# Kernel optimization log

Measured on AMD Instinct MI355X. Metric: run time of the kernel, lower is better.

## Reference

```python
import jax, jax.numpy as jnp
import numpy as np

B, C, K, D = 8192, 64, 256, 64  # batch, ncodebooks, ncentroids, subvect_len
BN_EPS = 1e-5


def setup_inputs() -> dict:
    key = jax.random.key(0)
    k1, k2 = jax.random.split(key)
    return {
        "inputs": jax.random.normal(k1, (B, C, D), dtype=jnp.float32),
        "centroids_k": jax.random.normal(k2, (C, K, D), dtype=jnp.float32) * 0.1,
        "bn_gamma": jnp.ones((C,), dtype=jnp.float32),
        "bn_beta": jnp.zeros((C,), dtype=jnp.float32),
    }


def _response(inputs, centroids_k, bn_gamma, bn_beta):
    # dot-metric scores: (B, C, K)
    r = jnp.einsum('bcd,ckd->bck', inputs, centroids_k)
    # BatchNorm1d over channel dim C (training mode: biased batch stats over B and K)
    mean = r.mean(axis=(0, 2), keepdims=True)
    var = ((r - mean) ** 2).mean(axis=(0, 2), keepdims=True)
    r = (r - mean) * jax.lax.rsqrt(var + BN_EPS)
    return r * bn_gamma[None, :, None] + bn_beta[None, :, None]


def reference(inputs, centroids_k, bn_gamma, bn_beta):
    r = _response(inputs, centroids_k, bn_gamma, bn_beta)
    # torch.max(response, -1) -> (values, indices)
    mse = r.max(axis=-1)                 # (B, C)
    codes = jnp.argmax(r, axis=-1)       # (B, C) int
    # tie_in_n_out=True: _centroids_v is _centroids_k
    return codes, mse, centroids_k
```

## Files before the change

kernel.cpp:

```cpp
#include <hip/hip_runtime.h>

#define B_  8192
#define C_  64
#define K_  256
#define D_  64
#define NBT     2
#define ROWS_BT 512
#define GX  (B_ / (ROWS_BT * NBT))
#define BC_ (B_ * C_)
#define BN_EPS 1e-5

#define WCAP_C 1024
#define DELTA  4e-3f

typedef _Float16 f16x8 __attribute__((ext_vector_type(8)));
typedef float    f32x4 __attribute__((ext_vector_type(4)));

__device__ __forceinline__ int swz(int row, int dbyte) {
    return (row * 128 + dbyte) ^ ((row & 7) << 4);
}

__device__ __forceinline__ f16x8 cvt8(const float* p) {
    float4 u0 = *(const float4*)p;
    float4 u1 = *(const float4*)(p + 4);
    return (f16x8){(_Float16)u0.x, (_Float16)u0.y, (_Float16)u0.z, (_Float16)u0.w,
                   (_Float16)u1.x, (_Float16)u1.y, (_Float16)u1.z, (_Float16)u1.w};
}

#define MERGE2(B1, S1, B2, S2)                                              \
    {                                                                       \
        const float lo_ = fminf(B1, B2);                                    \
        B1 = fmaxf(B1, B2);                                                 \
        S1 = fmaxf(lo_, fmaxf(S1, S2));                                     \
    }

__global__ __launch_bounds__(512, 4) void dpq_mfma(
    const float* __restrict__ x,
    const float* __restrict__ cent,
    const float* __restrict__ gamma,
    float* __restrict__ out,
    float* __restrict__ part_sum,
    float* __restrict__ part_sq,
    int* __restrict__ wcount,
    int* __restrict__ worklist)
{
    __shared__ char lds[32768];
    const int c   = blockIdx.y;
    const int tid = threadIdx.x;
    const float sgn = (gamma[c] < 0.0f) ? -1.0f : 1.0f;

    {
        const int row = tid >> 1, half = tid & 1;
        const float* g = cent + ((size_t)c * K_ + row) * D_ + half * 32;
#pragma unroll
        for (int q = 0; q < 4; ++q) {
            float v[8];
#pragma unroll
            for (int j = 0; j < 8; ++j) v[j] = g[q * 8 + j] * sgn;
            f16x8 h = {(_Float16)v[0], (_Float16)v[1], (_Float16)v[2], (_Float16)v[3],
                       (_Float16)v[4], (_Float16)v[5], (_Float16)v[6], (_Float16)v[7]};
            *(f16x8*)(lds + swz(row, half * 64 + q * 16)) = h;
        }
    }
    __syncthreads();

    const int wid = tid >> 6, lane = tid & 63;
    const int col = lane & 15, grp = lane >> 4;
    const unsigned g4 = (unsigned)(grp * 4);

    float taccs[4] = {0.f, 0.f, 0.f, 0.f};
    float taccq[4] = {0.f, 0.f, 0.f, 0.f};

    for (int bt = 0; bt < NBT; ++bt) {
        const int b0 = blockIdx.x * (ROWS_BT * NBT) + bt * ROWS_BT + wid * 64;

        f16x8 xfa[4], xfb[4];
        {
            const float* xb = x + ((size_t)(b0 + col) * C_ + c) * D_ + grp * 8;
            const size_t st16 = (size_t)16 * C_ * D_;
#pragma unroll
            for (int T = 0; T < 4; ++T) {
                xfa[T] = cvt8(xb + T * st16);
                xfb[T] = cvt8(xb + T * st16 + 32);
            }
        }

        float bestv[4], secv[4];
#pragma unroll
        for (int T = 0; T < 4; ++T) { bestv[T] = -3.4e38f; secv[T] = -3.4e38f; }

#pragma unroll 4
        for (int t = 0; t < 16; ++t) {
            const f16x8 a0 = *(const f16x8*)(lds + swz(t * 16 + col,      grp * 16));
            const f16x8 a1 = *(const f16x8*)(lds + swz(t * 16 + col, 64 + grp * 16));

            f32x4 p[4];
#pragma unroll
            for (int T = 0; T < 4; ++T) {
                f32x4 acc = {0.f, 0.f, 0.f, 0.f};
                acc = __builtin_amdgcn_mfma_f32_16x16x32_f16(a0, xfa[T], acc, 0, 0, 0);
                acc = __builtin_amdgcn_mfma_f32_16x16x32_f16(a1, xfb[T], acc, 0, 0, 0);
                p[T] = acc;
            }

            const unsigned kt = ((unsigned)t << 4) | g4;
#pragma unroll
            for (int j = 0; j < 4; ++j) {
                const unsigned kj = kt + j;
#pragma unroll
                for (int T = 0; T < 4; ++T) {
                    const float r = p[T][j];
                    taccs[T] += r;
                    taccq[T] = fmaf(r, r, taccq[T]);
                    const float pk = __uint_as_float(
                        (__float_as_uint(r) & 0xFFFFFF00u) | kj);
                    secv[T]  = __builtin_amdgcn_fmed3f(pk, bestv[T], secv[T]);
                    bestv[T] = fmaxf(bestv[T], pk);
                }
            }
        }

#pragma unroll
        for (int T = 0; T < 4; ++T) {
            float bv = bestv[T], sv = secv[T];
#pragma unroll
            for (int m = 16; m <= 32; m <<= 1) {
                const float ob = __shfl_xor(bv, m);
                const float os = __shfl_xor(sv, m);
                MERGE2(bv, sv, ob, os);
            }
            if (grp == 0) {
                const int b = b0 + T * 16 + col;
                const size_t idx = (size_t)b * C_ + c;
                const unsigned bits = __float_as_uint(bv);
                out[idx] = (float)(bits & 255u);
                out[(size_t)BC_ + idx] = __uint_as_float(bits & 0xFFFFFF00u);
                if (bv - sv < DELTA && worklist) {
                    const int slot = atomicAdd(&wcount[c], 1);
                    if (slot < WCAP_C) worklist[c * WCAP_C + slot] = b;
                }
            }
        }
    }

    float accs = (taccs[0] + taccs[1]) + (taccs[2] + taccs[3]);
    float accq = (taccq[0] + taccq[1]) + (taccq[2] + taccq[3]);
#pragma unroll
    for (int m = 1; m <= 32; m <<= 1) {
        accs += __shfl_xor(accs, m);
        accq += __shfl_xor(accq, m);
    }
    __syncthreads();
    float* red = (float*)lds;
    if (lane == 0) { red[wid] = accs; red[8 + wid] = accq; }
    __syncthreads();
    if (tid == 0) {
        float s = 0.f, q = 0.f;
#pragma unroll
        for (int w = 0; w < 8; ++w) { s += red[w]; q += red[8 + w]; }
        part_sum[c * GX + blockIdx.x] = s;
        part_sq [c * GX + blockIdx.x] = q;
    }
}

__global__ __launch_bounds__(256) void dpq_referee(
    const float* __restrict__ x,
    const float* __restrict__ cent,
    const float* __restrict__ gamma,
    const int* __restrict__ wcount,
    const int* __restrict__ worklist,
    float* __restrict__ out)
{
    __shared__ float cl[K_ * D_];
    const int c = blockIdx.x;
    int n = wcount[c];
    if (n > WCAP_C) n = WCAP_C;
    if (n == 0) return;
    const int t = threadIdx.x;
    const float sgnf = (gamma[c] < 0.0f) ? -1.0f : 1.0f;

    {
        const float* g = cent + ((size_t)c * K_ + t) * D_;
#pragma unroll 8
        for (int d = 0; d < D_; ++d)
            cl[t * D_ + (d ^ (t & 31))] = g[d];
    }
    __syncthreads();

    const int wid = t >> 6, lane = t & 63;
    for (int i = blockIdx.y * 4 + wid; i < n; i += gridDim.y * 4) {
        const int b = worklist[c * WCAP_C + i];
        const float* xr = x + ((size_t)b * C_ + c) * D_;
        double bv = -1.0e300;
        int bk = 0;
#pragma unroll
        for (int q = 0; q < 4; ++q) {
            const int k = q * 64 + lane;
            const int sw = k & 31;
            double s = 0.0;
#pragma unroll 8
            for (int d = 0; d < D_; ++d)
                s += (double)xr[d] * (double)cl[k * D_ + (d ^ sw)];
            s *= (double)sgnf;
            if (s > bv) { bv = s; bk = k; }
        }
#pragma unroll
        for (int m = 1; m <= 32; m <<= 1) {
            const double ov = __shfl_xor(bv, m);
            const int   ok = __shfl_xor(bk, m);
            if (ov > bv || (ov == bv && ok < bk)) { bv = ov; bk = ok; }
        }
        if (lane == 0) {
            const size_t idx = (size_t)b * C_ + c;
            out[idx] = (float)bk;
            out[(size_t)BC_ + idx] = (float)bv;
        }
    }
}

__global__ void dpq_stats(
    const float* __restrict__ part_sum,
    const float* __restrict__ part_sq,
    const float* __restrict__ gamma,
    const float* __restrict__ beta,
    float* __restrict__ scale_out,
    float* __restrict__ shift_out)
{
    const int c = threadIdx.x;
    if (c >= C_) return;
    double s = 0.0, q = 0.0;
    for (int i = 0; i < GX; ++i) {
        s += (double)part_sum[c * GX + i];
        q += (double)part_sq [c * GX + i];
    }
    const double n    = (double)B_ * (double)K_;
    const double mean = s / n;
    const double var  = q / n - mean * mean;
    const double sc   = fabs((double)gamma[c]) / sqrt(var + BN_EPS);
    scale_out[c] = (float)sc;
    shift_out[c] = (float)((double)beta[c] - mean * sc);
}

__global__ __launch_bounds__(256) void dpq_apply(
    float* __restrict__ out,
    const float* __restrict__ scale,
    const float* __restrict__ shift)
{
    const int idx = blockIdx.x * 256 + threadIdx.x;
    const int c = idx & (C_ - 1);
    const float sc = scale[c];
    const float sh = shift[c];
    if (sc == 0.0f) {
        out[idx] = 0.0f;
        out[(size_t)BC_ + idx] = sh;
    } else {
        out[(size_t)BC_ + idx] = fmaf(out[(size_t)BC_ + idx], sc, sh);
    }
}

extern "C" void kernel_launch(void* const* d_in, const int* in_sizes, int n_in,
                              void* d_out, int out_size, void* d_ws, size_t ws_size,
                              hipStream_t stream)
{
    const float* x     = (const float*)d_in[0];
    const float* cent  = (const float*)d_in[1];
    const float* gamma = (const float*)d_in[2];
    const float* beta  = (const float*)d_in[3];
    float* out = (float*)d_out;
    float* ws  = (float*)d_ws;

    float* part_sum = ws;
    float* part_sq  = ws + 512;
    float* scale    = ws + 1024;
    float* shift    = ws + 1088;
    int*   wcount   = (int*)(ws + 1152);
    int*   worklist = (int*)(ws + 1216);
    const size_t need = (size_t)(1216 + C_ * WCAP_C) * 4;
    if (ws_size < need) { wcount = nullptr; worklist = nullptr; }

    if (wcount)
        (void)hipMemsetAsync(wcount, 0, C_ * sizeof(int), stream);

    dim3 g1(GX, C_);
    hipLaunchKernelGGL(dpq_mfma, g1, dim3(512), 0, stream,
                       x, cent, gamma, out, part_sum, part_sq, wcount, worklist);
    if (wcount)
        hipLaunchKernelGGL(dpq_referee, dim3(C_, 8), dim3(256), 0, stream,
                           x, cent, gamma, wcount, worklist, out);
    hipLaunchKernelGGL(dpq_stats, dim3(1), dim3(64), 0, stream,
                       part_sum, part_sq, gamma, beta, scale, shift);
    hipLaunchKernelGGL(dpq_apply, dim3(BC_ / 256), dim3(256), 0, stream,
                       out, scale, shift);
    (void)hipMemcpyAsync(out + 2 * (size_t)BC_, cent,
                         (size_t)C_ * K_ * D_ * sizeof(float),
                         hipMemcpyDeviceToDevice, stream);
}
```

Before: 111.9 us.

## Compute batch-norm sum via centroid-sum MFMA and fuse stats, apply and copy

The per-element sum over K is replaced algebraically: a prep kernel sums the centroids over K, and one extra MFMA pair per tile gives x·csum, so the sum accumulation drops out of the inner loop. The memset is folded into the prep kernel, and the stats kernel and centroid memcpy are folded into the apply kernel to cut launches. The referee grid is halved and the ambiguity threshold DELTA is lowered. In exchange each apply block redundantly reduces the partials in double, and the sum now comes from fp16-rounded centroid sums, which may differ slightly from summing the scores directly.

```diff
diff --git a/kernel.cpp b/kernel.cpp
--- a/kernel.cpp
+++ b/kernel.cpp
@@ -11,7 +11,7 @@
 #define BN_EPS 1e-5
 
 #define WCAP_C 1024
-#define DELTA  4e-3f
+#define DELTA  2.5e-3f
 
 typedef _Float16 f16x8 __attribute__((ext_vector_type(8)));
 typedef float    f32x4 __attribute__((ext_vector_type(4)));
@@ -34,17 +34,31 @@
         S1 = fmaxf(lo_, fmaxf(S1, S2));                                     \
     }
 
+__global__ __launch_bounds__(64) void dpq_prep(
+    const float* __restrict__ cent, float* __restrict__ csum,
+    int* __restrict__ wcount)
+{
+    const int c = blockIdx.x, d = threadIdx.x;
+    const float* g = cent + (size_t)c * K_ * D_ + d;
+    float s = 0.f;
+#pragma unroll 8
+    for (int k = 0; k < K_; ++k) s += g[(size_t)k * D_];
+    csum[c * D_ + d] = s;
+    if (d == 0) wcount[c] = 0;
+}
+
 __global__ __launch_bounds__(512, 4) void dpq_mfma(
     const float* __restrict__ x,
     const float* __restrict__ cent,
     const float* __restrict__ gamma,
+    const float* __restrict__ csum,
     float* __restrict__ out,
     float* __restrict__ part_sum,
     float* __restrict__ part_sq,
     int* __restrict__ wcount,
     int* __restrict__ worklist)
 {
-    __shared__ char lds[32768];
+    __shared__ char lds[34816];
     const int c   = blockIdx.y;
     const int tid = threadIdx.x;
     const float sgn = (gamma[c] < 0.0f) ? -1.0f : 1.0f;
@@ -61,6 +75,16 @@
                        (_Float16)v[4], (_Float16)v[5], (_Float16)v[6], (_Float16)v[7]};
             *(f16x8*)(lds + swz(row, half * 64 + q * 16)) = h;
         }
+    }
+    if (tid < 128) {
+        const int row = tid >> 3, q = tid & 7;
+        f16x8 h = {0, 0, 0, 0, 0, 0, 0, 0};
+        if (row == 0) {
+            const float* cs = csum + c * D_ + q * 8;
+#pragma unroll
+            for (int j = 0; j < 8; ++j) h[j] = (_Float16)(cs[j] * sgn);
+        }
+        *(f16x8*)(lds + 32768 + swz(row, q * 16)) = h;
     }
     __syncthreads();
 
@@ -110,13 +134,24 @@
 #pragma unroll
                 for (int T = 0; T < 4; ++T) {
                     const float r = p[T][j];
-                    taccs[T] += r;
                     taccq[T] = fmaf(r, r, taccq[T]);
                     const float pk = __uint_as_float(
                         (__float_as_uint(r) & 0xFFFFFF00u) | kj);
                     secv[T]  = __builtin_amdgcn_fmed3f(pk, bestv[T], secv[T]);
                     bestv[T] = fmaxf(bestv[T], pk);
                 }
+            }
+        }
+
+        {
+            const f16x8 a0v = *(const f16x8*)(lds + 32768 + swz(col,      grp * 16));
+            const f16x8 a1v = *(const f16x8*)(lds + 32768 + swz(col, 64 + grp * 16));
+#pragma unroll
+            for (int T = 0; T < 4; ++T) {
+                f32x4 pv = {0.f, 0.f, 0.f, 0.f};
+                pv = __builtin_amdgcn_mfma_f32_16x16x32_f16(a0v, xfa[T], pv, 0, 0, 0);
+                pv = __builtin_amdgcn_mfma_f32_16x16x32_f16(a1v, xfb[T], pv, 0, 0, 0);
+                taccs[T] += pv[0];
             }
         }
 
@@ -175,7 +210,7 @@
     const int c = blockIdx.x;
     int n = wcount[c];
     if (n > WCAP_C) n = WCAP_C;
-    if (n == 0) return;
+    if (n <= 0) return;
     const int t = threadIdx.x;
     const float sgnf = (gamma[c] < 0.0f) ? -1.0f : 1.0f;
 
@@ -218,43 +253,45 @@
     }
 }
 
-__global__ void dpq_stats(
+__global__ __launch_bounds__(256) void dpq_apply(
+    float* __restrict__ out,
     const float* __restrict__ part_sum,
     const float* __restrict__ part_sq,
     const float* __restrict__ gamma,
     const float* __restrict__ beta,
-    float* __restrict__ scale_out,
-    float* __restrict__ shift_out)
-{
-    const int c = threadIdx.x;
-    if (c >= C_) return;
-    double s = 0.0, q = 0.0;
-    for (int i = 0; i < GX; ++i) {
-        s += (double)part_sum[c * GX + i];
-        q += (double)part_sq [c * GX + i];
-    }
-    const double n    = (double)B_ * (double)K_;
-    const double mean = s / n;
-    const double var  = q / n - mean * mean;
-    const double sc   = fabs((double)gamma[c]) / sqrt(var + BN_EPS);
-    scale_out[c] = (float)sc;
-    shift_out[c] = (float)((double)beta[c] - mean * sc);
-}
-
-__global__ __launch_bounds__(256) void dpq_apply(
-    float* __restrict__ out,
-    const float* __restrict__ scale,
-    const float* __restrict__ shift)
-{
-    const int idx = blockIdx.x * 256 + threadIdx.x;
+    const float* __restrict__ cent)
+{
+    __shared__ float sc_s[C_], sh_s[C_];
+    const int tid = threadIdx.x;
+    if (tid < C_) {
+        double s = 0.0, q = 0.0;
+#pragma unroll
+        for (int i = 0; i < GX; ++i) {
+            s += (double)part_sum[tid * GX + i];
+            q += (double)part_sq [tid * GX + i];
+        }
+        const double n    = (double)B_ * (double)K_;
+        const double mean = s / n;
+        const double var  = q / n - mean * mean;
+        const double sc   = fabs((double)gamma[tid]) / sqrt(var + BN_EPS);
+        sc_s[tid] = (float)sc;
+        sh_s[tid] = (float)((double)beta[tid] - mean * sc);
+    }
+    __syncthreads();
+
+    const int idx = blockIdx.x * 256 + tid;
     const int c = idx & (C_ - 1);
-    const float sc = scale[c];
-    const float sh = shift[c];
+    const float sc = sc_s[c];
+    const float sh = sh_s[c];
     if (sc == 0.0f) {
         out[idx] = 0.0f;
         out[(size_t)BC_ + idx] = sh;
     } else {
         out[(size_t)BC_ + idx] = fmaf(out[(size_t)BC_ + idx], sc, sh);
+    }
+
+    if (idx < (C_ * K_ * D_) / 4) {
+        ((float4*)(out + 2 * (size_t)BC_))[idx] = ((const float4*)cent)[idx];
     }
 }
 
@@ -269,29 +306,20 @@
     float* out = (float*)d_out;
     float* ws  = (float*)d_ws;
 
-    float* part_sum = ws;
-    float* part_sq  = ws + 512;
-    float* scale    = ws + 1024;
-    float* shift    = ws + 1088;
-    int*   wcount   = (int*)(ws + 1152);
-    int*   worklist = (int*)(ws + 1216);
-    const size_t need = (size_t)(1216 + C_ * WCAP_C) * 4;
-    if (ws_size < need) { wcount = nullptr; worklist = nullptr; }
-
-    if (wcount)
-        (void)hipMemsetAsync(wcount, 0, C_ * sizeof(int), stream);
-
+    float* csum     = ws;
+    float* part_sum = ws + 4096;
+    float* part_sq  = ws + 4608;
+    int*   wcount   = (int*)(ws + 5120);
+    int*   worklist = (int*)(ws + 5184);
+
+    hipLaunchKernelGGL(dpq_prep, dim3(C_), dim3(64), 0, stream,
+                       cent, csum, wcount);
     dim3 g1(GX, C_);
     hipLaunchKernelGGL(dpq_mfma, g1, dim3(512), 0, stream,
-                       x, cent, gamma, out, part_sum, part_sq, wcount, worklist);
-    if (wcount)
-        hipLaunchKernelGGL(dpq_referee, dim3(C_, 8), dim3(256), 0, stream,
-                           x, cent, gamma, wcount, worklist, out);
-    hipLaunchKernelGGL(dpq_stats, dim3(1), dim3(64), 0, stream,
-                       part_sum, part_sq, gamma, beta, scale, shift);
+                       x, cent, gamma, csum, out, part_sum, part_sq,
+                       wcount, worklist);
+    hipLaunchKernelGGL(dpq_referee, dim3(C_, 4), dim3(256), 0, stream,
+                       x, cent, gamma, wcount, worklist, out);
     hipLaunchKernelGGL(dpq_apply, dim3(BC_ / 256), dim3(256), 0, stream,
-                       out, scale, shift);
-    (void)hipMemcpyAsync(out + 2 * (size_t)BC_, cent,
-                         (size_t)C_ * K_ * D_ * sizeof(float),
-                         hipMemcpyDeviceToDevice, stream);
-}
+                       out, part_sum, part_sq, gamma, beta, cent);
+}
```

Result: faster. 100.6 us (-10.1%).
